# Kernel optimization log

Hardware: AMD Instinct MI355X
Metric: run time of the kernel (lower is better)

The kernel has to match this reference:

```python
import jax, jax.numpy as jnp
import numpy as np

N_HEADS = 16

def setup_inputs() -> dict:
    key = jax.random.key(0)
    ks = jax.random.split(key, 4)
    B, T, C = 2, 2048, 1024
    scale = 0.02
    return {
        "x": jax.random.normal(ks[0], (B, T, C), dtype=jnp.float32),
        "w_qkv": jax.random.normal(ks[1], (C, 3 * C), dtype=jnp.float32) * scale,
        "b_qkv": jnp.zeros((3 * C,), dtype=jnp.float32),
        "w_out": jax.random.normal(ks[2], (C, C), dtype=jnp.float32) * scale,
        "b_out": jnp.zeros((C,), dtype=jnp.float32),
    }

def reference(x, w_qkv, b_qkv, w_out, b_out):
    B, T, C = x.shape
    H = N_HEADS
    hd = C // H
    qkv = x @ w_qkv + b_qkv                      # [B,T,3C]
    q, k, v = jnp.split(qkv, 3, axis=-1)
    # [B,H,T,hd]
    q = q.reshape(B, T, H, hd).transpose(0, 2, 1, 3)
    k = k.reshape(B, T, H, hd).transpose(0, 2, 1, 3)
    v = v.reshape(B, T, H, hd).transpose(0, 2, 1, 3)
    att = jnp.einsum('bhqd,bhkd->bhqk', q, k) / jnp.sqrt(jnp.float32(hd))
    causal = jnp.tril(jnp.ones((T, T), dtype=bool))
    att = jnp.where(causal, att, -jnp.inf)
    att = jax.nn.softmax(att, axis=-1)
    # dropout is identity in eval mode (p effectively 0 for reference)
    y = jnp.einsum('bhqk,bhkd->bhqd', att, v)
    y = y.transpose(0, 2, 1, 3).reshape(B, T, C)
    return y @ w_out + b_out
```

## Files before the change

kernel.cpp:

```cpp
#include <hip/hip_runtime.h>
#include <hip/hip_bf16.h>

#define DEVI __device__ __forceinline__

typedef __attribute__((ext_vector_type(8))) short bf16x8_t;
typedef __attribute__((ext_vector_type(4))) float f32x4_t;
typedef __attribute__((ext_vector_type(4))) short s16x4_t;
typedef __attribute__((ext_vector_type(2))) unsigned int u32x2_t;

static DEVI unsigned short f2b_bits(float f) {
    unsigned int u = __float_as_uint(f);
    unsigned int r = (u + 0x7fffu + ((u >> 16) & 1u)) >> 16;
    return (unsigned short)r;
}

static DEVI unsigned int cvtpk_bf16(float lo, float hi) {
    unsigned int r;
    asm("v_cvt_pk_bf16_f32 %0, %1, %2" : "=v"(r) : "v"(lo), "v"(hi));
    return r;
}

static DEVI void gload16(const short* g, short* l) {
    __builtin_amdgcn_global_load_lds((const __attribute__((address_space(1))) void*)g,
                                     (__attribute__((address_space(3))) void*)l, 16, 0, 0);
}

__global__ void cast_bf16_k(const float* __restrict__ in, short* __restrict__ out, long n) {
    long i = ((long)blockIdx.x * blockDim.x + threadIdx.x) * 4;
    if (i >= n) return;
    const float4 v = *(const float4*)(in + i);
    s16x4_t o;
    o[0] = (short)f2b_bits(v.x); o[1] = (short)f2b_bits(v.y);
    o[2] = (short)f2b_bits(v.z); o[3] = (short)f2b_bits(v.w);
    *(s16x4_t*)(out + i) = o;
}

__global__ void transpose_cast(const float* __restrict__ w, short* __restrict__ wT,
                               int K, int N) {
    __shared__ float tile[32][33];
    const int n0 = blockIdx.x * 32, k0 = blockIdx.y * 32;
    const int tx = threadIdx.x, ty = threadIdx.y;
#pragma unroll
    for (int i = 0; i < 4; ++i)
        tile[ty + 8 * i][tx] = w[(long)(k0 + ty + 8 * i) * N + n0 + tx];
    __syncthreads();
#pragma unroll
    for (int i = 0; i < 4; ++i)
        wT[(long)(n0 + ty + 8 * i) * K + k0 + tx] = (short)f2b_bits(tile[tx][ty + 8 * i]);
}

template<int OUT_F32>
__global__ __launch_bounds__(256, 2) void gemm_bt(const short* __restrict__ A,
                                                  const short* __restrict__ Bt,
                                                  const float* __restrict__ bias,
                                                  void* __restrict__ Cv,
                                                  int M, int N, int K,
                                                  int qcols, float qscale) {
    __shared__ __align__(16) short lsA[128 * 32];
    __shared__ __align__(16) short lsB[128 * 32];
    const int tid = threadIdx.x;
    const int lane = tid & 63;
    const int w = tid >> 6;
    const int wr = w >> 1, wc = w & 1;
    const int l15 = lane & 15, lg = lane >> 4;
    const long m0 = (long)blockIdx.y * 128;
    const long n0 = (long)blockIdx.x * 128;

    f32x4_t acc[4][4] = {};

    const int srow = tid >> 2;
    const int scol = (tid & 3) * 8;
    const short* gA = A + (m0 + srow) * (long)K + scol;
    const short* gB = Bt + (n0 + srow) * (long)K + scol;
    short* lA = lsA + tid * 8;
    short* lB = lsB + tid * 8;

    for (int kt = 0; kt < K; kt += 32) {
        __syncthreads();
        gload16(gA + kt, lA);
        gload16(gA + kt + (long)64 * K, lA + 2048);
        gload16(gB + kt, lB);
        gload16(gB + kt + (long)64 * K, lB + 2048);
        __syncthreads();
        bf16x8_t af[4], bfr[4];
#pragma unroll
        for (int m = 0; m < 4; ++m)
            af[m] = *(const bf16x8_t*)&lsA[(wr * 64 + m * 16 + l15) * 32 + lg * 8];
#pragma unroll
        for (int n = 0; n < 4; ++n)
            bfr[n] = *(const bf16x8_t*)&lsB[(wc * 64 + n * 16 + l15) * 32 + lg * 8];
#pragma unroll
        for (int m = 0; m < 4; ++m)
#pragma unroll
            for (int n = 0; n < 4; ++n)
                acc[m][n] = __builtin_amdgcn_mfma_f32_16x16x32_bf16(af[m], bfr[n], acc[m][n], 0, 0, 0);
    }

#pragma unroll
    for (int n = 0; n < 4; ++n) {
        const long col = n0 + wc * 64 + n * 16 + l15;
        const float bv = bias[col];
        const float sc = (col < qcols) ? qscale : 1.0f;
#pragma unroll
        for (int m = 0; m < 4; ++m) {
            const long row = m0 + wr * 64 + m * 16 + lg * 4;
#pragma unroll
            for (int j = 0; j < 4; ++j) {
                float v = (acc[m][n][j] + bv) * sc;
                if (OUT_F32) ((float*)Cv)[(row + j) * N + col] = v;
                else         ((short*)Cv)[(row + j) * N + col] = (short)f2b_bits(v);
            }
        }
    }
}

__global__ __launch_bounds__(256) void vtrans(const short* __restrict__ qkv,
                                              short* __restrict__ vt) {
    __shared__ __align__(16) short tile[64][72];
    const int bh = blockIdx.x >> 5, ti = blockIdx.x & 31;
    const int b = bh >> 4, h = bh & 15;
    const int tid = threadIdx.x;
    const int srow = tid >> 3;
    const int scol = (tid & 7) * 8;
#pragma unroll
    for (int p = 0; p < 2; ++p) {
        const int r = srow + 32 * p;
        *(bf16x8_t*)&tile[r][scol] =
            *(const bf16x8_t*)&qkv[((long)b * 2048 + ti * 64 + r) * 3072 + 2048 + h * 64 + scol];
    }
    __syncthreads();
#pragma unroll
    for (int p = 0; p < 2; ++p) {
        const int hd = srow + 32 * p;
        const int tc = scol;
        bf16x8_t v;
#pragma unroll
        for (int i = 0; i < 8; ++i) v[i] = tile[tc + i][hd];
        *(bf16x8_t*)&vt[((long)bh * 64 + hd) * 2048 + ti * 64 + tc] = v;
    }
}

__global__ __launch_bounds__(256, 4) void attn_fwd(const short* __restrict__ qkv,
                                                   const short* __restrict__ vt,
                                                   short* __restrict__ y) {
    __shared__ __align__(16) short lsK[2][64 * 64];
    __shared__ __align__(16) short lsV[2][64 * 64];
    __shared__ __align__(16) short lsP[4 * 16 * 64];
    const int bid = blockIdx.x;
    const int bh = bid & 31;
    const int t = bid >> 5;
    const int qi = (t < 16) ? t : 47 - t;
    const int b = bh >> 4, h = bh & 15;
    const int tid = threadIdx.x, w = tid >> 6, lane = tid & 63;
    const int l15 = lane & 15, lg = lane >> 4;
    const int lg4 = lg * 4;
    const int swz = (l15 & 7) << 4;

    const long qrow = (long)qi * 64 + w * 16 + l15;
    const bf16x8_t qf0 = *(const bf16x8_t*)&qkv[((long)b * 2048 + qrow) * 3072 + h * 64 + lg * 8];
    const bf16x8_t qf1 = *(const bf16x8_t*)&qkv[((long)b * 2048 + qrow) * 3072 + h * 64 + 32 + lg * 8];

    const int srow = tid >> 3;
    const int scolb = (tid & 7) * 16;
    const int sc = (scolb ^ ((srow & 7) << 4)) >> 1;
    const short* gK = qkv + ((long)b * 2048 + srow) * 3072 + 1024 + h * 64 + sc;
    const short* gV = vt + ((long)bh * 64 + srow) * 2048 + sc;

    auto STAGE = [&](int jt, int bufi) {
        const short* k0 = gK + (long)jt * 64 * 3072;
        const short* v0 = gV + (long)jt * 64;
        gload16(k0,              &lsK[bufi][tid * 8]);
        gload16(k0 + 32 * 3072,  &lsK[bufi][tid * 8 + 2048]);
        gload16(v0,              &lsV[bufi][tid * 8]);
        gload16(v0 + 32 * 2048,  &lsV[bufi][tid * 8 + 2048]);
    };

    float mrow = -3e38f, lrow = 0.f;
    f32x4_t oacc[4] = {};

    STAGE(0, 0);
    __syncthreads();
    int buf = 0;

    for (int j = 0; j <= qi; ++j) {
        if (j < qi) STAGE(j + 1, buf ^ 1);
        const bool diag = (j == qi);
        const char* Kb = (const char*)lsK[buf];
        const char* Vb = (const char*)lsV[buf];

        f32x4_t s[4] = {};
        const int nlim = diag ? (w + 1) : 4;
#pragma unroll
        for (int kq = 0; kq < 2; ++kq) {
            const bf16x8_t qf = kq ? qf1 : qf0;
#pragma unroll
            for (int n = 0; n < 4; ++n) {
                if (n < nlim) {
                    bf16x8_t kf = *(const bf16x8_t*)(Kb + (n * 16 + l15) * 128 + ((kq * 64 + lg * 16) ^ swz));
                    s[n] = __builtin_amdgcn_mfma_f32_16x16x32_bf16(kf, qf, s[n], 0, 0, 0);
                }
            }
        }

        float p[4][4];
#pragma unroll
        for (int n = 0; n < 4; ++n)
#pragma unroll
            for (int r = 0; r < 4; ++r) p[n][r] = s[n][r];

        if (diag) {
            const int ql = w * 16 + l15 - lg4;
#pragma unroll
            for (int n = 0; n < 4; ++n)
#pragma unroll
                for (int r = 0; r < 4; ++r)
                    if (n * 16 + r > ql) p[n][r] = -3e38f;
        }

        float pm = -3e38f;
#pragma unroll
        for (int n = 0; n < 4; ++n)
            pm = fmaxf(pm, fmaxf(fmaxf(p[n][0], p[n][1]), fmaxf(p[n][2], p[n][3])));
        pm = fmaxf(pm, __shfl_xor(pm, 16));
        pm = fmaxf(pm, __shfl_xor(pm, 32));

        const float mnew = fmaxf(mrow, pm);
        const float alpha = __expf(mrow - mnew);
        mrow = mnew;

        float lsum = 0.f;
#pragma unroll
        for (int n = 0; n < 4; ++n)
#pragma unroll
            for (int r = 0; r < 4; ++r) {
                p[n][r] = __expf(p[n][r] - mnew);
                lsum += p[n][r];
            }
        lsum += __shfl_xor(lsum, 16);
        lsum += __shfl_xor(lsum, 32);
        lrow = lrow * alpha + lsum;

        char* Pb = (char*)lsP + w * 2048 + l15 * 128;
#pragma unroll
        for (int n = 0; n < 4; ++n) {
            u32x2_t dw;
            dw[0] = cvtpk_bf16(p[n][0], p[n][1]);
            dw[1] = cvtpk_bf16(p[n][2], p[n][3]);
            *(u32x2_t*)(Pb + ((n * 32 + lg * 8) ^ swz)) = dw;
        }

        float ar[4];
#pragma unroll
        for (int r = 0; r < 4; ++r) ar[r] = __shfl(alpha, lg4 + r);
#pragma unroll
        for (int n = 0; n < 4; ++n)
#pragma unroll
            for (int r = 0; r < 4; ++r) oacc[n][r] *= ar[r];

        asm volatile("s_waitcnt lgkmcnt(0)" ::: "memory");

#pragma unroll
        for (int kk = 0; kk < 2; ++kk) {
            if (!(diag && kk * 32 > w * 16 + 15)) {
                bf16x8_t pf = *(const bf16x8_t*)(Pb + ((kk * 64 + lg * 16) ^ swz));
#pragma unroll
                for (int n = 0; n < 4; ++n) {
                    bf16x8_t vf = *(const bf16x8_t*)(Vb + (n * 16 + l15) * 128 + ((kk * 64 + lg * 16) ^ swz));
                    oacc[n] = __builtin_amdgcn_mfma_f32_16x16x32_bf16(pf, vf, oacc[n], 0, 0, 0);
                }
            }
        }
        __syncthreads();
        buf ^= 1;
    }

    float lr[4];
#pragma unroll
    for (int r = 0; r < 4; ++r) lr[r] = 1.0f / __shfl(lrow, lg4 + r);
#pragma unroll
    for (int n = 0; n < 4; ++n)
#pragma unroll
        for (int r = 0; r < 4; ++r) {
            const float ov = oacc[n][r] * lr[r];
            y[((long)b * 2048 + qi * 64 + w * 16 + lg4 + r) * 1024 + h * 64 + n * 16 + l15] =
                (short)f2b_bits(ov);
        }
}

extern "C" void kernel_launch(void* const* d_in, const int* in_sizes, int n_in,
                              void* d_out, int out_size, void* d_ws, size_t ws_size,
                              hipStream_t stream) {
    const float* x     = (const float*)d_in[0];
    const float* w_qkv = (const float*)d_in[1];
    const float* b_qkv = (const float*)d_in[2];
    const float* w_out = (const float*)d_in[3];
    const float* b_out = (const float*)d_in[4];

    char* ws = (char*)d_ws;
    size_t off = 0;
    short* xb    = (short*)(ws + off); off += (size_t)4096 * 1024 * 2;
    short* wqkvT = (short*)(ws + off); off += (size_t)3072 * 1024 * 2;
    short* woutT = (short*)(ws + off); off += (size_t)1024 * 1024 * 2;
    short* qkvb  = (short*)(ws + off); off += (size_t)4096 * 3072 * 2;
    short* vt    = (short*)(ws + off); off += (size_t)32 * 64 * 2048 * 2;
    short* yatt  = (short*)(ws + off); off += (size_t)4096 * 1024 * 2;

    cast_bf16_k<<<4096, 256, 0, stream>>>(x, xb, 4194304L);
    transpose_cast<<<dim3(96, 32), dim3(32, 8), 0, stream>>>(w_qkv, wqkvT, 1024, 3072);
    transpose_cast<<<dim3(32, 32), dim3(32, 8), 0, stream>>>(w_out, woutT, 1024, 1024);
    gemm_bt<0><<<dim3(24, 32), 256, 0, stream>>>(xb, wqkvT, b_qkv, (void*)qkvb, 4096, 3072, 1024, 1024, 0.125f);
    vtrans<<<1024, 256, 0, stream>>>(qkvb, vt);
    attn_fwd<<<1024, 256, 0, stream>>>(qkvb, vt, yatt);
    gemm_bt<1><<<dim3(8, 32), 256, 0, stream>>>(yatt, woutT, b_out, d_out, 4096, 1024, 1024, 0, 1.0f);
}
```

Measured before the change: 194.9 us.

## Fuse V transpose into QKV GEMM, enlarge attention Q tile, use exp2 softmax

The QKV GEMM epilogue now writes V directly in transposed per-head layout, which removes the separate vtrans kernel and its extra read and write of V. The attention kernel handles 128 query rows per block, with each wave owning 32 rows, so every staged K/V tile feeds twice the MFMA work, and the launch drops to 512 blocks. Q is prescaled by log2(e)/sqrt(hd) so softmax can use exp2. The running-max rescale is skipped unless the max grows by more than 8. These changes add register pressure (occupancy hint lowered to 2) and change how causal load balance is spread across blocks.

```diff
diff --git a/kernel.cpp b/kernel.cpp
--- a/kernel.cpp
+++ b/kernel.cpp
@@ -7,6 +7,9 @@
 typedef __attribute__((ext_vector_type(4))) float f32x4_t;
 typedef __attribute__((ext_vector_type(4))) short s16x4_t;
 typedef __attribute__((ext_vector_type(2))) unsigned int u32x2_t;
+
+#define QSCALE 0.18033688011112043f
+#define EXP2F(x) __builtin_amdgcn_exp2f(x)
 
 static DEVI unsigned short f2b_bits(float f) {
     unsigned int u = __float_as_uint(f);
@@ -49,13 +52,13 @@
         wT[(long)(n0 + ty + 8 * i) * K + k0 + tx] = (short)f2b_bits(tile[tx][ty + 8 * i]);
 }
 
-template<int OUT_F32>
+template<int MODE>
 __global__ __launch_bounds__(256, 2) void gemm_bt(const short* __restrict__ A,
                                                   const short* __restrict__ Bt,
                                                   const float* __restrict__ bias,
                                                   void* __restrict__ Cv,
-                                                  int M, int N, int K,
-                                                  int qcols, float qscale) {
+                                                  short* __restrict__ vtp,
+                                                  int M, int N, int K) {
     __shared__ __align__(16) short lsA[128 * 32];
     __shared__ __align__(16) short lsB[128 * 32];
     const int tid = threadIdx.x;
@@ -98,67 +101,66 @@
 
 #pragma unroll
     for (int n = 0; n < 4; ++n) {
-        const long col = n0 + wc * 64 + n * 16 + l15;
+        const int col = (int)n0 + wc * 64 + n * 16 + l15;
         const float bv = bias[col];
-        const float sc = (col < qcols) ? qscale : 1.0f;
-#pragma unroll
-        for (int m = 0; m < 4; ++m) {
-            const long row = m0 + wr * 64 + m * 16 + lg * 4;
-#pragma unroll
-            for (int j = 0; j < 4; ++j) {
-                float v = (acc[m][n][j] + bv) * sc;
-                if (OUT_F32) ((float*)Cv)[(row + j) * N + col] = v;
-                else         ((short*)Cv)[(row + j) * N + col] = (short)f2b_bits(v);
+        if (MODE == 1) {
+#pragma unroll
+            for (int m = 0; m < 4; ++m) {
+                const long row = m0 + wr * 64 + m * 16 + lg * 4;
+#pragma unroll
+                for (int j = 0; j < 4; ++j)
+                    ((float*)Cv)[(row + j) * N + col] = acc[m][n][j] + bv;
+            }
+        } else if (col < 2048) {
+            const float sc = (col < 1024) ? QSCALE : 1.0f;
+#pragma unroll
+            for (int m = 0; m < 4; ++m) {
+                const long row = m0 + wr * 64 + m * 16 + lg * 4;
+#pragma unroll
+                for (int j = 0; j < 4; ++j)
+                    ((short*)Cv)[(row + j) * N + col] = (short)f2b_bits((acc[m][n][j] + bv) * sc);
+            }
+        } else {
+            const int hc = col - 2048;
+            const int hh = hc >> 6, dd = hc & 63;
+#pragma unroll
+            for (int m = 0; m < 4; ++m) {
+                const long row = m0 + wr * 64 + m * 16 + lg * 4;
+                const int bb = (int)(row >> 11), tt = (int)(row & 2047);
+                s16x4_t pk;
+#pragma unroll
+                for (int j = 0; j < 4; ++j) pk[j] = (short)f2b_bits(acc[m][n][j] + bv);
+                *(s16x4_t*)&vtp[((long)(bb * 16 + hh) * 64 + dd) * 2048 + tt] = pk;
             }
         }
     }
 }
 
-__global__ __launch_bounds__(256) void vtrans(const short* __restrict__ qkv,
-                                              short* __restrict__ vt) {
-    __shared__ __align__(16) short tile[64][72];
-    const int bh = blockIdx.x >> 5, ti = blockIdx.x & 31;
-    const int b = bh >> 4, h = bh & 15;
-    const int tid = threadIdx.x;
-    const int srow = tid >> 3;
-    const int scol = (tid & 7) * 8;
-#pragma unroll
-    for (int p = 0; p < 2; ++p) {
-        const int r = srow + 32 * p;
-        *(bf16x8_t*)&tile[r][scol] =
-            *(const bf16x8_t*)&qkv[((long)b * 2048 + ti * 64 + r) * 3072 + 2048 + h * 64 + scol];
-    }
-    __syncthreads();
-#pragma unroll
-    for (int p = 0; p < 2; ++p) {
-        const int hd = srow + 32 * p;
-        const int tc = scol;
-        bf16x8_t v;
-#pragma unroll
-        for (int i = 0; i < 8; ++i) v[i] = tile[tc + i][hd];
-        *(bf16x8_t*)&vt[((long)bh * 64 + hd) * 2048 + ti * 64 + tc] = v;
-    }
-}
-
-__global__ __launch_bounds__(256, 4) void attn_fwd(const short* __restrict__ qkv,
+__global__ __launch_bounds__(256, 2) void attn_fwd(const short* __restrict__ qkv,
                                                    const short* __restrict__ vt,
                                                    short* __restrict__ y) {
     __shared__ __align__(16) short lsK[2][64 * 64];
     __shared__ __align__(16) short lsV[2][64 * 64];
-    __shared__ __align__(16) short lsP[4 * 16 * 64];
+    __shared__ __align__(16) short lsP[4 * 32 * 64];
     const int bid = blockIdx.x;
     const int bh = bid & 31;
     const int t = bid >> 5;
-    const int qi = (t < 16) ? t : 47 - t;
+    const int qi = (t < 8) ? (15 - 2 * t) : (2 * (t - 8));
+    const int iters = 2 * qi + 2;
     const int b = bh >> 4, h = bh & 15;
     const int tid = threadIdx.x, w = tid >> 6, lane = tid & 63;
-    const int l15 = lane & 15, lg = lane >> 4;
-    const int lg4 = lg * 4;
+    const int l15 = lane & 15, lg = lane >> 4, lg4 = lg * 4;
     const int swz = (l15 & 7) << 4;
 
-    const long qrow = (long)qi * 64 + w * 16 + l15;
-    const bf16x8_t qf0 = *(const bf16x8_t*)&qkv[((long)b * 2048 + qrow) * 3072 + h * 64 + lg * 8];
-    const bf16x8_t qf1 = *(const bf16x8_t*)&qkv[((long)b * 2048 + qrow) * 3072 + h * 64 + 32 + lg * 8];
+    const int qmin = qi * 128 + w * 32;
+
+    bf16x8_t qf[2][2];
+#pragma unroll
+    for (int qq = 0; qq < 2; ++qq)
+#pragma unroll
+        for (int kq = 0; kq < 2; ++kq)
+            qf[qq][kq] = *(const bf16x8_t*)&qkv[((long)b * 2048 + qmin + qq * 16 + l15) * 3072 +
+                                                h * 64 + kq * 32 + lg * 8];
 
     const int srow = tid >> 3;
     const int scolb = (tid & 7) * 16;
@@ -169,104 +171,134 @@
     auto STAGE = [&](int jt, int bufi) {
         const short* k0 = gK + (long)jt * 64 * 3072;
         const short* v0 = gV + (long)jt * 64;
-        gload16(k0,              &lsK[bufi][tid * 8]);
-        gload16(k0 + 32 * 3072,  &lsK[bufi][tid * 8 + 2048]);
-        gload16(v0,              &lsV[bufi][tid * 8]);
-        gload16(v0 + 32 * 2048,  &lsV[bufi][tid * 8 + 2048]);
+        gload16(k0,             &lsK[bufi][tid * 8]);
+        gload16(k0 + 32 * 3072, &lsK[bufi][tid * 8 + 2048]);
+        gload16(v0,             &lsV[bufi][tid * 8]);
+        gload16(v0 + 32 * 2048, &lsV[bufi][tid * 8 + 2048]);
     };
 
-    float mrow = -3e38f, lrow = 0.f;
-    f32x4_t oacc[4] = {};
+    float mrow[2] = {-3e38f, -3e38f}, lrow[2] = {0.f, 0.f};
+    f32x4_t oacc[2][4] = {};
 
     STAGE(0, 0);
     __syncthreads();
     int buf = 0;
 
-    for (int j = 0; j <= qi; ++j) {
-        if (j < qi) STAGE(j + 1, buf ^ 1);
-        const bool diag = (j == qi);
-        const char* Kb = (const char*)lsK[buf];
-        const char* Vb = (const char*)lsV[buf];
-
-        f32x4_t s[4] = {};
-        const int nlim = diag ? (w + 1) : 4;
-#pragma unroll
-        for (int kq = 0; kq < 2; ++kq) {
-            const bf16x8_t qf = kq ? qf1 : qf0;
-#pragma unroll
-            for (int n = 0; n < 4; ++n) {
-                if (n < nlim) {
-                    bf16x8_t kf = *(const bf16x8_t*)(Kb + (n * 16 + l15) * 128 + ((kq * 64 + lg * 16) ^ swz));
-                    s[n] = __builtin_amdgcn_mfma_f32_16x16x32_bf16(kf, qf, s[n], 0, 0, 0);
+    for (int j = 0; j < iters; ++j) {
+        if (j + 1 < iters) STAGE(j + 1, buf ^ 1);
+        const int kv0 = j * 64;
+        if (kv0 <= qmin + 31) {
+            const char* Kb = (const char*)lsK[buf];
+            const char* Vb = (const char*)lsV[buf];
+            const int base0 = qmin - kv0;
+            const bool needmask = (base0 < 63);
+            int nlim0 = 4, nlim1 = 4;
+            if (needmask) {
+                nlim0 = min(4, ((base0 + 15) >> 4) + 1);
+                nlim1 = min(4, ((base0 + 31) >> 4) + 1);
+            }
+
+            f32x4_t s[2][4] = {};
+#pragma unroll
+            for (int kq = 0; kq < 2; ++kq)
+#pragma unroll
+                for (int n = 0; n < 4; ++n)
+                    if (n < nlim1) {
+                        bf16x8_t kf = *(const bf16x8_t*)(Kb + (n * 16 + l15) * 128 +
+                                                         ((kq * 64 + lg * 16) ^ swz));
+                        s[1][n] = __builtin_amdgcn_mfma_f32_16x16x32_bf16(kf, qf[1][kq], s[1][n], 0, 0, 0);
+                        if (n < nlim0)
+                            s[0][n] = __builtin_amdgcn_mfma_f32_16x16x32_bf16(kf, qf[0][kq], s[0][n], 0, 0, 0);
+                    }
+
+            float p[2][4][4];
+#pragma unroll
+            for (int qq = 0; qq < 2; ++qq)
+#pragma unroll
+                for (int n = 0; n < 4; ++n)
+#pragma unroll
+                    for (int r = 0; r < 4; ++r) p[qq][n][r] = s[qq][n][r];
+
+            if (needmask) {
+#pragma unroll
+                for (int qq = 0; qq < 2; ++qq) {
+                    const int qb = base0 + qq * 16 + l15;
+#pragma unroll
+                    for (int n = 0; n < 4; ++n)
+#pragma unroll
+                        for (int r = 0; r < 4; ++r)
+                            if (n * 16 + lg4 + r > qb) p[qq][n][r] = -3e38f;
                 }
             }
-        }
-
-        float p[4][4];
-#pragma unroll
-        for (int n = 0; n < 4; ++n)
-#pragma unroll
-            for (int r = 0; r < 4; ++r) p[n][r] = s[n][r];
-
-        if (diag) {
-            const int ql = w * 16 + l15 - lg4;
-#pragma unroll
-            for (int n = 0; n < 4; ++n)
-#pragma unroll
-                for (int r = 0; r < 4; ++r)
-                    if (n * 16 + r > ql) p[n][r] = -3e38f;
-        }
-
-        float pm = -3e38f;
-#pragma unroll
-        for (int n = 0; n < 4; ++n)
-            pm = fmaxf(pm, fmaxf(fmaxf(p[n][0], p[n][1]), fmaxf(p[n][2], p[n][3])));
-        pm = fmaxf(pm, __shfl_xor(pm, 16));
-        pm = fmaxf(pm, __shfl_xor(pm, 32));
-
-        const float mnew = fmaxf(mrow, pm);
-        const float alpha = __expf(mrow - mnew);
-        mrow = mnew;
-
-        float lsum = 0.f;
-#pragma unroll
-        for (int n = 0; n < 4; ++n)
-#pragma unroll
-            for (int r = 0; r < 4; ++r) {
-                p[n][r] = __expf(p[n][r] - mnew);
-                lsum += p[n][r];
-            }
-        lsum += __shfl_xor(lsum, 16);
-        lsum += __shfl_xor(lsum, 32);
-        lrow = lrow * alpha + lsum;
-
-        char* Pb = (char*)lsP + w * 2048 + l15 * 128;
-#pragma unroll
-        for (int n = 0; n < 4; ++n) {
-            u32x2_t dw;
-            dw[0] = cvtpk_bf16(p[n][0], p[n][1]);
-            dw[1] = cvtpk_bf16(p[n][2], p[n][3]);
-            *(u32x2_t*)(Pb + ((n * 32 + lg * 8) ^ swz)) = dw;
-        }
-
-        float ar[4];
-#pragma unroll
-        for (int r = 0; r < 4; ++r) ar[r] = __shfl(alpha, lg4 + r);
-#pragma unroll
-        for (int n = 0; n < 4; ++n)
-#pragma unroll
-            for (int r = 0; r < 4; ++r) oacc[n][r] *= ar[r];
-
-        asm volatile("s_waitcnt lgkmcnt(0)" ::: "memory");
-
-#pragma unroll
-        for (int kk = 0; kk < 2; ++kk) {
-            if (!(diag && kk * 32 > w * 16 + 15)) {
-                bf16x8_t pf = *(const bf16x8_t*)(Pb + ((kk * 64 + lg * 16) ^ swz));
+
+            float pm[2];
+#pragma unroll
+            for (int qq = 0; qq < 2; ++qq) {
+                float v = -3e38f;
+#pragma unroll
+                for (int n = 0; n < 4; ++n)
+                    v = fmaxf(v, fmaxf(fmaxf(p[qq][n][0], p[qq][n][1]),
+                                       fmaxf(p[qq][n][2], p[qq][n][3])));
+                v = fmaxf(v, __shfl_xor(v, 16));
+                v = fmaxf(v, __shfl_xor(v, 32));
+                pm[qq] = v;
+            }
+
+            if (!__all((pm[0] <= mrow[0] + 8.f) && (pm[1] <= mrow[1] + 8.f))) {
+#pragma unroll
+                for (int qq = 0; qq < 2; ++qq) {
+                    const float mnew = fmaxf(mrow[qq], pm[qq]);
+                    const float al = EXP2F(mrow[qq] - mnew);
+                    mrow[qq] = mnew;
+                    lrow[qq] *= al;
+                    float ar[4];
+#pragma unroll
+                    for (int r = 0; r < 4; ++r) ar[r] = __shfl(al, lg4 + r);
+#pragma unroll
+                    for (int n = 0; n < 4; ++n)
+#pragma unroll
+                        for (int r = 0; r < 4; ++r) oacc[qq][n][r] *= ar[r];
+                }
+            }
+
+#pragma unroll
+            for (int qq = 0; qq < 2; ++qq) {
+                float lsum = 0.f;
+                char* Pb = (char*)lsP + w * 4096 + (qq * 16 + l15) * 128;
 #pragma unroll
                 for (int n = 0; n < 4; ++n) {
-                    bf16x8_t vf = *(const bf16x8_t*)(Vb + (n * 16 + l15) * 128 + ((kk * 64 + lg * 16) ^ swz));
-                    oacc[n] = __builtin_amdgcn_mfma_f32_16x16x32_bf16(pf, vf, oacc[n], 0, 0, 0);
+#pragma unroll
+                    for (int r = 0; r < 4; ++r) {
+                        const float pv = EXP2F(p[qq][n][r] - mrow[qq]);
+                        lsum += pv;
+                        p[qq][n][r] = pv;
+                    }
+                    u32x2_t dw;
+                    dw[0] = cvtpk_bf16(p[qq][n][0], p[qq][n][1]);
+                    dw[1] = cvtpk_bf16(p[qq][n][2], p[qq][n][3]);
+                    *(u32x2_t*)(Pb + ((n * 32 + lg * 8) ^ swz)) = dw;
+                }
+                lsum += __shfl_xor(lsum, 16);
+                lsum += __shfl_xor(lsum, 32);
+                lrow[qq] += lsum;
+            }
+
+            asm volatile("s_waitcnt lgkmcnt(0)" ::: "memory");
+
+#pragma unroll
+            for (int kk = 0; kk < 2; ++kk) {
+                if (kv0 + kk * 32 <= qmin + 31) {
+                    bf16x8_t pf0 = *(const bf16x8_t*)((char*)lsP + w * 4096 + l15 * 128 +
+                                                      ((kk * 64 + lg * 16) ^ swz));
+                    bf16x8_t pf1 = *(const bf16x8_t*)((char*)lsP + w * 4096 + (16 + l15) * 128 +
+                                                      ((kk * 64 + lg * 16) ^ swz));
+#pragma unroll
+                    for (int n = 0; n < 4; ++n) {
+                        bf16x8_t vf = *(const bf16x8_t*)(Vb + (n * 16 + l15) * 128 +
+                                                         ((kk * 64 + lg * 16) ^ swz));
+                        oacc[0][n] = __builtin_amdgcn_mfma_f32_16x16x32_bf16(pf0, vf, oacc[0][n], 0, 0, 0);
+                        oacc[1][n] = __builtin_amdgcn_mfma_f32_16x16x32_bf16(pf1, vf, oacc[1][n], 0, 0, 0);
+                    }
                 }
             }
         }
@@ -274,17 +306,18 @@
         buf ^= 1;
     }
 
-    float lr[4];
-#pragma unroll
-    for (int r = 0; r < 4; ++r) lr[r] = 1.0f / __shfl(lrow, lg4 + r);
-#pragma unroll
-    for (int n = 0; n < 4; ++n)
-#pragma unroll
-        for (int r = 0; r < 4; ++r) {
-            const float ov = oacc[n][r] * lr[r];
-            y[((long)b * 2048 + qi * 64 + w * 16 + lg4 + r) * 1024 + h * 64 + n * 16 + l15] =
-                (short)f2b_bits(ov);
-        }
+#pragma unroll
+    for (int qq = 0; qq < 2; ++qq) {
+        float lr[4];
+#pragma unroll
+        for (int r = 0; r < 4; ++r) lr[r] = 1.0f / __shfl(lrow[qq], lg4 + r);
+#pragma unroll
+        for (int n = 0; n < 4; ++n)
+#pragma unroll
+            for (int r = 0; r < 4; ++r)
+                y[((long)b * 2048 + qmin + qq * 16 + lg4 + r) * 1024 + h * 64 + n * 16 + l15] =
+                    (short)f2b_bits(oacc[qq][n][r] * lr[r]);
+    }
 }
 
 extern "C" void kernel_launch(void* const* d_in, const int* in_sizes, int n_in,
@@ -308,8 +341,7 @@
     cast_bf16_k<<<4096, 256, 0, stream>>>(x, xb, 4194304L);
     transpose_cast<<<dim3(96, 32), dim3(32, 8), 0, stream>>>(w_qkv, wqkvT, 1024, 3072);
     transpose_cast<<<dim3(32, 32), dim3(32, 8), 0, stream>>>(w_out, woutT, 1024, 1024);
-    gemm_bt<0><<<dim3(24, 32), 256, 0, stream>>>(xb, wqkvT, b_qkv, (void*)qkvb, 4096, 3072, 1024, 1024, 0.125f);
-    vtrans<<<1024, 256, 0, stream>>>(qkvb, vt);
-    attn_fwd<<<1024, 256, 0, stream>>>(qkvb, vt, yatt);
-    gemm_bt<1><<<dim3(8, 32), 256, 0, stream>>>(yatt, woutT, b_out, d_out, 4096, 1024, 1024, 0, 1.0f);
-}
+    gemm_bt<0><<<dim3(24, 32), 256, 0, stream>>>(xb, wqkvT, b_qkv, (void*)qkvb, vt, 4096, 3072, 1024);
+    attn_fwd<<<512, 256, 0, stream>>>(qkvb, vt, yatt);
+    gemm_bt<1><<<dim3(8, 32), 256, 0, stream>>>(yatt, woutT, b_out, d_out, nullptr, 4096, 1024, 1024);
+}
```

Result: slower. 206.6 us (+6.0%).

## Fuse V transpose into QKV GEMM epilogue, double-buffer GEMM, lazy softmax rescale

Applied to the files above, without the earlier changes.

The QKV GEMM epilogue now writes the V columns straight into the transposed per-head layout, which removes the separate vtrans kernel and its extra global read and write. The GEMM main loop is double-buffered in LDS with a single barrier per k-step, and s_setprio is raised around the MFMA blocks in both the GEMM and attention kernels. Attention switches to exp2 by folding log2(e) into the Q scale, and skips rescaling the running output unless the row max grows by more than a threshold. The lazy rescale trades a small amount of numerical headroom (unnormalized values up to 2^8) for fewer exponentials and multiplies on the common path.

```diff
diff --git a/kernel.cpp b/kernel.cpp
--- a/kernel.cpp
+++ b/kernel.cpp
@@ -7,6 +7,9 @@
 typedef __attribute__((ext_vector_type(4))) float f32x4_t;
 typedef __attribute__((ext_vector_type(4))) short s16x4_t;
 typedef __attribute__((ext_vector_type(2))) unsigned int u32x2_t;
+
+#define QSCALE 0.18033688011112043f
+#define EXP2F(x) __builtin_amdgcn_exp2f(x)
 
 static DEVI unsigned short f2b_bits(float f) {
     unsigned int u = __float_as_uint(f);
@@ -49,15 +52,15 @@
         wT[(long)(n0 + ty + 8 * i) * K + k0 + tx] = (short)f2b_bits(tile[tx][ty + 8 * i]);
 }
 
-template<int OUT_F32>
+template<int MODE>
 __global__ __launch_bounds__(256, 2) void gemm_bt(const short* __restrict__ A,
                                                   const short* __restrict__ Bt,
                                                   const float* __restrict__ bias,
                                                   void* __restrict__ Cv,
-                                                  int M, int N, int K,
-                                                  int qcols, float qscale) {
-    __shared__ __align__(16) short lsA[128 * 32];
-    __shared__ __align__(16) short lsB[128 * 32];
+                                                  short* __restrict__ vtp,
+                                                  int M, int N, int K) {
+    __shared__ __align__(16) short lsA[2][128 * 32];
+    __shared__ __align__(16) short lsB[2][128 * 32];
     const int tid = threadIdx.x;
     const int lane = tid & 63;
     const int w = tid >> 6;
@@ -72,71 +75,73 @@
     const int scol = (tid & 3) * 8;
     const short* gA = A + (m0 + srow) * (long)K + scol;
     const short* gB = Bt + (n0 + srow) * (long)K + scol;
-    short* lA = lsA + tid * 8;
-    short* lB = lsB + tid * 8;
-
-    for (int kt = 0; kt < K; kt += 32) {
-        __syncthreads();
-        gload16(gA + kt, lA);
-        gload16(gA + kt + (long)64 * K, lA + 2048);
-        gload16(gB + kt, lB);
-        gload16(gB + kt + (long)64 * K, lB + 2048);
-        __syncthreads();
+
+    auto STAGE = [&](int kt, int bi) {
+        gload16(gA + kt,                &lsA[bi][tid * 8]);
+        gload16(gA + kt + (long)64 * K, &lsA[bi][tid * 8 + 2048]);
+        gload16(gB + kt,                &lsB[bi][tid * 8]);
+        gload16(gB + kt + (long)64 * K, &lsB[bi][tid * 8 + 2048]);
+    };
+
+    const int nt = K >> 5;
+    STAGE(0, 0);
+    __syncthreads();
+    int buf = 0;
+
+    for (int i = 0; i < nt; ++i) {
+        if (i + 1 < nt) STAGE((i + 1) << 5, buf ^ 1);
         bf16x8_t af[4], bfr[4];
 #pragma unroll
         for (int m = 0; m < 4; ++m)
-            af[m] = *(const bf16x8_t*)&lsA[(wr * 64 + m * 16 + l15) * 32 + lg * 8];
+            af[m] = *(const bf16x8_t*)&lsA[buf][(wr * 64 + m * 16 + l15) * 32 + lg * 8];
 #pragma unroll
         for (int n = 0; n < 4; ++n)
-            bfr[n] = *(const bf16x8_t*)&lsB[(wc * 64 + n * 16 + l15) * 32 + lg * 8];
+            bfr[n] = *(const bf16x8_t*)&lsB[buf][(wc * 64 + n * 16 + l15) * 32 + lg * 8];
+        __builtin_amdgcn_s_setprio(1);
 #pragma unroll
         for (int m = 0; m < 4; ++m)
 #pragma unroll
             for (int n = 0; n < 4; ++n)
                 acc[m][n] = __builtin_amdgcn_mfma_f32_16x16x32_bf16(af[m], bfr[n], acc[m][n], 0, 0, 0);
+        __builtin_amdgcn_s_setprio(0);
+        __syncthreads();
+        buf ^= 1;
     }
 
 #pragma unroll
     for (int n = 0; n < 4; ++n) {
-        const long col = n0 + wc * 64 + n * 16 + l15;
+        const int col = (int)n0 + wc * 64 + n * 16 + l15;
         const float bv = bias[col];
-        const float sc = (col < qcols) ? qscale : 1.0f;
-#pragma unroll
-        for (int m = 0; m < 4; ++m) {
-            const long row = m0 + wr * 64 + m * 16 + lg * 4;
-#pragma unroll
-            for (int j = 0; j < 4; ++j) {
-                float v = (acc[m][n][j] + bv) * sc;
-                if (OUT_F32) ((float*)Cv)[(row + j) * N + col] = v;
-                else         ((short*)Cv)[(row + j) * N + col] = (short)f2b_bits(v);
-            }
-        }
-    }
-}
-
-__global__ __launch_bounds__(256) void vtrans(const short* __restrict__ qkv,
-                                              short* __restrict__ vt) {
-    __shared__ __align__(16) short tile[64][72];
-    const int bh = blockIdx.x >> 5, ti = blockIdx.x & 31;
-    const int b = bh >> 4, h = bh & 15;
-    const int tid = threadIdx.x;
-    const int srow = tid >> 3;
-    const int scol = (tid & 7) * 8;
-#pragma unroll
-    for (int p = 0; p < 2; ++p) {
-        const int r = srow + 32 * p;
-        *(bf16x8_t*)&tile[r][scol] =
-            *(const bf16x8_t*)&qkv[((long)b * 2048 + ti * 64 + r) * 3072 + 2048 + h * 64 + scol];
-    }
-    __syncthreads();
-#pragma unroll
-    for (int p = 0; p < 2; ++p) {
-        const int hd = srow + 32 * p;
-        const int tc = scol;
-        bf16x8_t v;
-#pragma unroll
-        for (int i = 0; i < 8; ++i) v[i] = tile[tc + i][hd];
-        *(bf16x8_t*)&vt[((long)bh * 64 + hd) * 2048 + ti * 64 + tc] = v;
+        if (MODE == 1) {
+#pragma unroll
+            for (int m = 0; m < 4; ++m) {
+                const long row = m0 + wr * 64 + m * 16 + lg * 4;
+#pragma unroll
+                for (int j = 0; j < 4; ++j)
+                    ((float*)Cv)[(row + j) * N + col] = acc[m][n][j] + bv;
+            }
+        } else if (col < 2048) {
+            const float sc = (col < 1024) ? QSCALE : 1.0f;
+#pragma unroll
+            for (int m = 0; m < 4; ++m) {
+                const long row = m0 + wr * 64 + m * 16 + lg * 4;
+#pragma unroll
+                for (int j = 0; j < 4; ++j)
+                    ((short*)Cv)[(row + j) * N + col] = (short)f2b_bits((acc[m][n][j] + bv) * sc);
+            }
+        } else {
+            const int hc = col - 2048;
+            const int hh = hc >> 6, dd = hc & 63;
+#pragma unroll
+            for (int m = 0; m < 4; ++m) {
+                const long row = m0 + wr * 64 + m * 16 + lg * 4;
+                const int bb = (int)(row >> 11), tt = (int)(row & 2047);
+                s16x4_t pk;
+#pragma unroll
+                for (int j = 0; j < 4; ++j) pk[j] = (short)f2b_bits(acc[m][n][j] + bv);
+                *(s16x4_t*)&vtp[((long)(bb * 16 + hh) * 64 + dd) * 2048 + tt] = pk;
+            }
+        }
     }
 }
 
@@ -169,10 +174,10 @@
     auto STAGE = [&](int jt, int bufi) {
         const short* k0 = gK + (long)jt * 64 * 3072;
         const short* v0 = gV + (long)jt * 64;
-        gload16(k0,              &lsK[bufi][tid * 8]);
-        gload16(k0 + 32 * 3072,  &lsK[bufi][tid * 8 + 2048]);
-        gload16(v0,              &lsV[bufi][tid * 8]);
-        gload16(v0 + 32 * 2048,  &lsV[bufi][tid * 8 + 2048]);
+        gload16(k0,             &lsK[bufi][tid * 8]);
+        gload16(k0 + 32 * 3072, &lsK[bufi][tid * 8 + 2048]);
+        gload16(v0,             &lsV[bufi][tid * 8]);
+        gload16(v0 + 32 * 2048, &lsV[bufi][tid * 8 + 2048]);
     };
 
     float mrow = -3e38f, lrow = 0.f;
@@ -190,6 +195,7 @@
 
         f32x4_t s[4] = {};
         const int nlim = diag ? (w + 1) : 4;
+        __builtin_amdgcn_s_setprio(1);
 #pragma unroll
         for (int kq = 0; kq < 2; ++kq) {
             const bf16x8_t qf = kq ? qf1 : qf0;
@@ -201,6 +207,7 @@
                 }
             }
         }
+        __builtin_amdgcn_s_setprio(0);
 
         float p[4][4];
 #pragma unroll
@@ -224,41 +231,41 @@
         pm = fmaxf(pm, __shfl_xor(pm, 16));
         pm = fmaxf(pm, __shfl_xor(pm, 32));
 
-        const float mnew = fmaxf(mrow, pm);
-        const float alpha = __expf(mrow - mnew);
-        mrow = mnew;
+        if (!__all(pm <= mrow + 8.f)) {
+            const float mnew = fmaxf(mrow, pm);
+            const float al = EXP2F(mrow - mnew);
+            mrow = mnew;
+            lrow *= al;
+            float ar[4];
+#pragma unroll
+            for (int r = 0; r < 4; ++r) ar[r] = __shfl(al, lg4 + r);
+#pragma unroll
+            for (int n = 0; n < 4; ++n)
+#pragma unroll
+                for (int r = 0; r < 4; ++r) oacc[n][r] *= ar[r];
+        }
 
         float lsum = 0.f;
-#pragma unroll
-        for (int n = 0; n < 4; ++n)
+        char* Pb = (char*)lsP + w * 2048 + l15 * 128;
+#pragma unroll
+        for (int n = 0; n < 4; ++n) {
 #pragma unroll
             for (int r = 0; r < 4; ++r) {
-                p[n][r] = __expf(p[n][r] - mnew);
+                p[n][r] = EXP2F(p[n][r] - mrow);
                 lsum += p[n][r];
             }
-        lsum += __shfl_xor(lsum, 16);
-        lsum += __shfl_xor(lsum, 32);
-        lrow = lrow * alpha + lsum;
-
-        char* Pb = (char*)lsP + w * 2048 + l15 * 128;
-#pragma unroll
-        for (int n = 0; n < 4; ++n) {
             u32x2_t dw;
             dw[0] = cvtpk_bf16(p[n][0], p[n][1]);
             dw[1] = cvtpk_bf16(p[n][2], p[n][3]);
             *(u32x2_t*)(Pb + ((n * 32 + lg * 8) ^ swz)) = dw;
         }
-
-        float ar[4];
-#pragma unroll
-        for (int r = 0; r < 4; ++r) ar[r] = __shfl(alpha, lg4 + r);
-#pragma unroll
-        for (int n = 0; n < 4; ++n)
-#pragma unroll
-            for (int r = 0; r < 4; ++r) oacc[n][r] *= ar[r];
+        lsum += __shfl_xor(lsum, 16);
+        lsum += __shfl_xor(lsum, 32);
+        lrow += lsum;
 
         asm volatile("s_waitcnt lgkmcnt(0)" ::: "memory");
 
+        __builtin_amdgcn_s_setprio(1);
 #pragma unroll
         for (int kk = 0; kk < 2; ++kk) {
             if (!(diag && kk * 32 > w * 16 + 15)) {
@@ -270,6 +277,7 @@
                 }
             }
         }
+        __builtin_amdgcn_s_setprio(0);
         __syncthreads();
         buf ^= 1;
     }
@@ -308,8 +316,7 @@
     cast_bf16_k<<<4096, 256, 0, stream>>>(x, xb, 4194304L);
     transpose_cast<<<dim3(96, 32), dim3(32, 8), 0, stream>>>(w_qkv, wqkvT, 1024, 3072);
     transpose_cast<<<dim3(32, 32), dim3(32, 8), 0, stream>>>(w_out, woutT, 1024, 1024);
-    gemm_bt<0><<<dim3(24, 32), 256, 0, stream>>>(xb, wqkvT, b_qkv, (void*)qkvb, 4096, 3072, 1024, 1024, 0.125f);
-    vtrans<<<1024, 256, 0, stream>>>(qkvb, vt);
+    gemm_bt<0><<<dim3(24, 32), 256, 0, stream>>>(xb, wqkvT, b_qkv, (void*)qkvb, vt, 4096, 3072, 1024);
     attn_fwd<<<1024, 256, 0, stream>>>(qkvb, vt, yatt);
-    gemm_bt<1><<<dim3(8, 32), 256, 0, stream>>>(yatt, woutT, b_out, d_out, 4096, 1024, 1024, 0, 1.0f);
-}
+    gemm_bt<1><<<dim3(8, 32), 256, 0, stream>>>(yatt, woutT, b_out, d_out, nullptr, 4096, 1024, 1024);
+}
```

New measurement: 188.3 us. 3.4% less time.
